# Kernel optimization log

Hardware: AMD Instinct MI355X
Metric: run time of the kernel (lower is better)

The kernel has to match this reference:

```python
import jax, jax.numpy as jnp
import numpy as np

H = W = 32
V = 1.5  # gaussian sigma used by the original _gussin(1.5)

def _gaussian_table():
    # gus[p, x, y] with p = i*32 + k, matching the original nested loops.
    r = np.arange(H, dtype=np.float64)
    d = (r[:, None, None, None] - r[None, None, :, None]) ** 2 \
        + (r[None, :, None, None] - r[None, None, None, :]) ** 2  # [i,k,x,y]
    g = np.exp(-d / (2.0 * V * V)) / (2.0 * np.pi * V * V)
    g = g.reshape(H * W, H, W)
    g = g / g.sum(axis=(1, 2), keepdims=True)  # per-position boundary normalization
    return jnp.asarray(g, dtype=jnp.float32)

_GUS = _gaussian_table()  # [1024, 32, 32]

def setup_inputs() -> dict:
    key = jax.random.key(0)
    ks = jax.random.split(key, 5)
    c, r = 1024, 16
    return {
        "x": jax.random.normal(ks[0], (1, c, H, W), jnp.float32),
        "se_w1": jax.random.normal(ks[1], (c // r, c), jnp.float32) * 0.03,
        "se_b1": jnp.zeros((c // r,), jnp.float32),
        "se_w2": jax.random.normal(ks[2], (c, c // r), jnp.float32) * 0.1,
        "se_b2": jnp.zeros((c,), jnp.float32),
        "conv_w": jax.random.normal(ks[3], (c, 2 * c), jnp.float32) * 0.02,
        "bn_gamma": jnp.ones((c,), jnp.float32),
        "bn_beta": jnp.zeros((c,), jnp.float32),
        "bn_mean": jnp.zeros((c,), jnp.float32),
        "bn_var": jnp.ones((c,), jnp.float32),
    }

def reference(x, se_w1, se_b1, se_w2, se_b2, conv_w, bn_gamma, bn_beta, bn_mean, bn_var):
    b, c, h, w = x.shape  # b == 1, h == w == 32 (hardcoded by the gaussian table)
    # ---- SE block ----
    y = x.mean(axis=(2, 3))                              # [b, c]
    y = jax.nn.relu(y @ se_w1.T + se_b1)                 # [b, c//r]
    y = jax.nn.sigmoid(y @ se_w2.T + se_b2)              # [b, c]
    x = x * y[:, :, None, None]
    # ---- gaussian spatial pooling (algebraic form of the O(H^2 W^2 C) expand) ----
    # x_spatial[c, p] = sum_{h,w} x[c,h,w] * gus[p,h,w]
    x_spatial = jnp.einsum('chw,phw->cp', x[0], _GUS).reshape(c, h, w)
    # ---- 3x3 local softmax attention on sigmoid features ----
    xr = jax.nn.sigmoid(x)                               # [1, c, h, w]
    xp = jnp.pad(xr, ((0, 0), (0, 0), (1, 1), (1, 1)))
    # torch F.unfold ordering: feature index = c_idx*9 + kh*3 + kw
    patches = jnp.stack([xp[:, :, i:i + h, j:j + w]
                         for i in range(3) for j in range(3)], axis=2)  # [1, c, 9, h, w]
    u = patches.reshape(c * 9, h * w).T                  # [hw, c*9]
    # faithful to the original reshape(hw, 3, 3, c) (reinterprets the c*9 layout)
    x3 = u.reshape(h * w, 3, 3, c)
    x1 = xr[0].transpose(1, 2, 0).reshape(h * w, 1, 1, c)
    logits = (x1 * x3).sum(-1).reshape(h * w, 9)         # [hw, 9]
    attn = jax.nn.softmax(logits, axis=1).reshape(h * w, 3, 3)
    x_range = jnp.einsum('pij,pijc->cp', attn, x3).reshape(c, h, w)
    # ---- fuse: 1x1 conv (no bias) + eval-mode BatchNorm + ReLU ----
    cat = jnp.concatenate([x_range, x_spatial], axis=0).reshape(b, 2 * c, h, w)
    out = jnp.einsum('oc,bchw->bohw', conv_w, cat)
    inv = jax.lax.rsqrt(bn_var + 1e-5)
    out = (out - bn_mean[None, :, None, None]) * (inv * bn_gamma)[None, :, None, None] \
          + bn_beta[None, :, None, None]
    return jax.nn.relu(out)
```

## Files before the change

kernel.cpp:

```cpp
#include <hip/hip_runtime.h>
#include <hip/hip_bf16.h>


typedef __attribute__((ext_vector_type(8))) short v8s;
typedef __attribute__((ext_vector_type(4))) float v4f;

__device__ __forceinline__ float sigmoidf_(float v) {
    return 1.f / (1.f + __expf(-v));
}
__device__ __forceinline__ unsigned short f2bf(float f) {
    unsigned u = __float_as_uint(f);
    u += 0x7fffu + ((u >> 16) & 1u);
    return (unsigned short)(u >> 16);
}
__device__ __forceinline__ float bf2f(unsigned short s) {
    return __uint_as_float(((unsigned)s) << 16);
}

__global__ __launch_bounds__(256) void k_A(const float* __restrict__ x,
                                           const float* __restrict__ W,
                                           float* __restrict__ mean,
                                           unsigned short* __restrict__ Wb,
                                           unsigned short* __restrict__ K2,
                                           unsigned short* __restrict__ xb) {
    __shared__ float Gs[32][32];
    int tid = threadIdx.x, bx = blockIdx.x;
    int wv = tid >> 6, lane = tid & 63;
    {
        int row = tid >> 3, col0 = (tid & 7) << 2;
        float e[4], s = 0.f;
        #pragma unroll
        for (int j = 0; j < 4; ++j) {
            float d = (float)(row - (col0 + j));
            e[j] = __expf(-d * d / 4.5f);
            s += e[j];
        }
        s += __shfl_xor(s, 4, 8);
        s += __shfl_xor(s, 2, 8);
        s += __shfl_xor(s, 1, 8);
        float is = 1.f / s;
        #pragma unroll
        for (int j = 0; j < 4; ++j) Gs[row][col0 + j] = e[j] * is;
    }
    #pragma unroll
    for (int k = 0; k < 8; ++k) {
        int e = (k << 18) + (bx << 10) + (tid << 2);
        float4 v = *(const float4*)(W + e);
        uint2 pk;
        pk.x = (unsigned)f2bf(v.x) | ((unsigned)f2bf(v.y) << 16);
        pk.y = (unsigned)f2bf(v.z) | ((unsigned)f2bf(v.w) << 16);
        *(uint2*)(Wb + e) = pk;
    }
    int c = (bx << 2) + wv;
    const float* xp = x + (size_t)c * 1024;
    float4 vj[4];
    float s = 0.f;
    #pragma unroll
    for (int j = 0; j < 4; ++j) {
        vj[j] = *(const float4*)(xp + (j << 8) + (lane << 2));
        s += vj[j].x + vj[j].y + vj[j].z + vj[j].w;
    }
    #pragma unroll
    for (int o = 32; o; o >>= 1) s += __shfl_down(s, o);
    if (lane == 0) mean[c] = s * (1.f / 1024.f);
    #pragma unroll
    for (int j = 0; j < 4; ++j) {
        uint2 pk;
        pk.x = (unsigned)f2bf(vj[j].x) | ((unsigned)f2bf(vj[j].y) << 16);
        pk.y = (unsigned)f2bf(vj[j].z) | ((unsigned)f2bf(vj[j].w) << 16);
        *(uint2*)(xb + (size_t)c * 1024 + (j << 8) + (lane << 2)) = pk;
    }
    __syncthreads();
    {
        int p = (bx << 2) + wv;
        float gr = Gs[p >> 5][lane >> 1];
        const float* gq = &Gs[p & 31][(lane & 1) << 4];
        unsigned pk[8];
        #pragma unroll
        for (int t = 0; t < 8; ++t) {
            float v0 = gr * gq[2 * t];
            float v1 = gr * gq[2 * t + 1];
            pk[t] = (unsigned)f2bf(v0) | ((unsigned)f2bf(v1) << 16);
        }
        unsigned short* dst = K2 + (size_t)p * 1024 + (lane << 4);
        *(uint4*)dst = *(uint4*)&pk[0];
        *(uint4*)(dst + 8) = *(uint4*)&pk[4];
    }
}

__global__ __launch_bounds__(256) void k_prep(const float* __restrict__ x,
                                              const float* __restrict__ mean,
                                              const float* __restrict__ w1,
                                              const float* __restrict__ b1,
                                              const float* __restrict__ w2,
                                              const float* __restrict__ b2,
                                              unsigned short* __restrict__ xrb,
                                              float* __restrict__ y2out) {
    __shared__ float ms[1024];
    __shared__ float y1s[64];
    __shared__ float y2s[64];
    __shared__ float T[64][65];
    int tid = threadIdx.x;
    int p0 = blockIdx.x << 6, c0 = blockIdx.y << 6;
    *(float4*)&ms[tid << 2] = *(const float4*)(mean + (tid << 2));
    __syncthreads();
    int wv = tid >> 6, lane = tid & 63;
    #pragma unroll
    for (int jj = 0; jj < 16; ++jj) {
        int j = (wv << 4) + jj;
        float s = 0.f;
        #pragma unroll
        for (int kk = 0; kk < 4; ++kk) {
            float4 wv4 = *(const float4*)(w1 + (size_t)j * 1024 + kk * 256 + (lane << 2));
            float4 mv  = *(const float4*)&ms[kk * 256 + (lane << 2)];
            s += wv4.x * mv.x + wv4.y * mv.y + wv4.z * mv.z + wv4.w * mv.w;
        }
        #pragma unroll
        for (int o = 32; o; o >>= 1) s += __shfl_down(s, o);
        if (lane == 0) y1s[j] = fmaxf(s + b1[j], 0.f);
    }
    __syncthreads();
    {
        int ci = tid >> 2, sub = tid & 3;
        float s = 0.f;
        const float* w2r = w2 + (size_t)(c0 + ci) * 64 + sub * 16;
        #pragma unroll
        for (int i = 0; i < 4; ++i) {
            float4 wv4 = *(const float4*)(w2r + (i << 2));
            float4 yv4 = *(const float4*)&y1s[sub * 16 + (i << 2)];
            s += wv4.x * yv4.x + wv4.y * yv4.y + wv4.z * yv4.z + wv4.w * yv4.w;
        }
        s += __shfl_down(s, 2, 4);
        s += __shfl_down(s, 1, 4);
        if (sub == 0) y2s[ci] = sigmoidf_(s + b2[c0 + ci]);
    }
    __syncthreads();
    if (blockIdx.x == 0 && tid < 64) y2out[c0 + tid] = y2s[tid];
    #pragma unroll
    for (int i = 0; i < 4; ++i) {
        int idx = tid + (i << 8);
        int row = idx >> 4;
        int col = (idx & 15) << 2;
        float sc = y2s[row];
        float4 v = *(const float4*)(x + (size_t)(c0 + row) * 1024 + p0 + col);
        T[col + 0][row] = sigmoidf_(v.x * sc);
        T[col + 1][row] = sigmoidf_(v.y * sc);
        T[col + 2][row] = sigmoidf_(v.z * sc);
        T[col + 3][row] = sigmoidf_(v.w * sc);
    }
    __syncthreads();
    #pragma unroll
    for (int i = 0; i < 4; ++i) {
        int idx = tid + (i << 8);
        int prow = idx >> 4;
        int cc = (idx & 15) << 2;
        uint2 pk;
        pk.x = (unsigned)f2bf(T[prow][cc + 0]) | ((unsigned)f2bf(T[prow][cc + 1]) << 16);
        pk.y = (unsigned)f2bf(T[prow][cc + 2]) | ((unsigned)f2bf(T[prow][cc + 3]) << 16);
        *(uint2*)(xrb + (size_t)(p0 + prow) * 1024 + c0 + cc) = pk;
    }
}

union __align__(16) SMem {
    struct { unsigned short As[64 * 72]; unsigned short Bs[64 * 72]; } sp;
    struct { unsigned short val[9216]; float part[9][4]; } at;
};

__global__ __launch_bounds__(256) void k_spattn(const unsigned short* __restrict__ xb,
                                                const unsigned short* __restrict__ xrb,
                                                const unsigned short* __restrict__ K2,
                                                const float* __restrict__ y2,
                                                unsigned short* __restrict__ Bt) {
    __shared__ SMem sm;
    int tid = threadIdx.x;
    int bx = blockIdx.x;
    int wv = tid >> 6, lane = tid & 63;
    if (bx < 256) {
        int wm = wv & 1, wn = wv >> 1;
        int m0 = (bx >> 4) << 6, n0 = (bx & 15) << 6;
        int col = lane & 15, quad = lane >> 4;
        int smi = tid >> 2;
        int sg = (tid & 3) * 2;
        v4f acc[2][2];
        #pragma unroll
        for (int i = 0; i < 2; ++i)
            #pragma unroll
            for (int j = 0; j < 2; ++j) acc[i][j] = (v4f){0.f, 0.f, 0.f, 0.f};
        const float4* pa = (const float4*)(K2 + (size_t)(m0 + smi) * 1024 + sg * 8);
        const float4* pb = (const float4*)(xb + (size_t)(n0 + smi) * 1024 + sg * 8);
        float4 ka0 = pa[0], ka1 = pa[1];
        float4 kb0 = pb[0], kb1 = pb[1];
        for (int it = 0; it < 16; ++it) {
            __syncthreads();
            *(float4*)&sm.sp.As[smi * 72 + sg * 8] = ka0;
            *(float4*)&sm.sp.As[smi * 72 + sg * 8 + 8] = ka1;
            *(float4*)&sm.sp.Bs[smi * 72 + sg * 8] = kb0;
            *(float4*)&sm.sp.Bs[smi * 72 + sg * 8 + 8] = kb1;
            __syncthreads();
            if (it + 1 < 16) {
                int k0 = (it + 1) << 6;
                pa = (const float4*)(K2 + (size_t)(m0 + smi) * 1024 + k0 + sg * 8);
                pb = (const float4*)(xb + (size_t)(n0 + smi) * 1024 + k0 + sg * 8);
                ka0 = pa[0]; ka1 = pa[1];
                kb0 = pb[0]; kb1 = pb[1];
            }
            #pragma unroll
            for (int ks = 0; ks < 2; ++ks) {
                int kg = ks * 4 + quad;
                int rA = wm * 32 + col;
                int rB = wn * 32 + col;
                v8s a0 = *(const v8s*)&sm.sp.As[rA * 72 + kg * 8];
                v8s a1 = *(const v8s*)&sm.sp.As[(rA + 16) * 72 + kg * 8];
                v8s b0 = *(const v8s*)&sm.sp.Bs[rB * 72 + kg * 8];
                v8s b1 = *(const v8s*)&sm.sp.Bs[(rB + 16) * 72 + kg * 8];
                acc[0][0] = __builtin_amdgcn_mfma_f32_16x16x32_bf16(a0, b0, acc[0][0], 0, 0, 0);
                acc[0][1] = __builtin_amdgcn_mfma_f32_16x16x32_bf16(a0, b1, acc[0][1], 0, 0, 0);
                acc[1][0] = __builtin_amdgcn_mfma_f32_16x16x32_bf16(a1, b0, acc[1][0], 0, 0, 0);
                acc[1][1] = __builtin_amdgcn_mfma_f32_16x16x32_bf16(a1, b1, acc[1][1], 0, 0, 0);
            }
        }
        #pragma unroll
        for (int mi = 0; mi < 2; ++mi)
            #pragma unroll
            for (int ni = 0; ni < 2; ++ni) {
                int mb = m0 + wm * 32 + mi * 16 + quad * 4;
                int nn = n0 + wn * 32 + ni * 16 + col;
                float yv = y2[nn];
                #pragma unroll
                for (int r = 0; r < 4; ++r)
                    Bt[(size_t)(mb + r) * 2048 + 1024 + nn] = f2bf(acc[mi][ni][r] * yv);
            }
    } else {
        int p = bx - 256;
        int h = p >> 5, w = p & 31;
        #pragma unroll
        for (int rem = 0; rem < 9; ++rem) {
            int dh = rem / 3 - 1, dw = rem % 3 - 1;
            bool ok = ((unsigned)(h + dh) < 32u) && ((unsigned)(w + dw) < 32u);
            const unsigned short* rp = xrb + (size_t)((h + dh) * 32 + (w + dw)) * 1024;
            #pragma unroll
            for (int j = 0; j < 4; ++j) {
                int cf = tid + (j << 8);
                sm.at.val[cf * 9 + rem] = ok ? rp[cf] : (unsigned short)0;
            }
        }
        __syncthreads();
        float ctr[4], vvq[9][4], lg[9];
        #pragma unroll
        for (int j = 0; j < 4; ++j) ctr[j] = bf2f(sm.at.val[(4 * tid + j) * 9 + 4]);
        #pragma unroll
        for (int q = 0; q < 9; ++q) {
            uint2 pk = *(const uint2*)&sm.at.val[(q << 10) + 4 * tid];
            vvq[q][0] = bf2f((unsigned short)(pk.x & 0xffffu));
            vvq[q][1] = bf2f((unsigned short)(pk.x >> 16));
            vvq[q][2] = bf2f((unsigned short)(pk.y & 0xffffu));
            vvq[q][3] = bf2f((unsigned short)(pk.y >> 16));
            lg[q] = ctr[0] * vvq[q][0] + ctr[1] * vvq[q][1]
                  + ctr[2] * vvq[q][2] + ctr[3] * vvq[q][3];
        }
        #pragma unroll
        for (int q = 0; q < 9; ++q) {
            float s = lg[q];
            #pragma unroll
            for (int o = 32; o; o >>= 1) s += __shfl_down(s, o);
            if (lane == 0) sm.at.part[q][wv] = s;
        }
        __syncthreads();
        float a9[9], mx = -3.4e38f;
        #pragma unroll
        for (int q = 0; q < 9; ++q) {
            a9[q] = sm.at.part[q][0] + sm.at.part[q][1] + sm.at.part[q][2] + sm.at.part[q][3];
            mx = fmaxf(mx, a9[q]);
        }
        float se = 0.f;
        #pragma unroll
        for (int q = 0; q < 9; ++q) { a9[q] = __expf(a9[q] - mx); se += a9[q]; }
        float inv = 1.f / se;
        float o4[4] = {0.f, 0.f, 0.f, 0.f};
        #pragma unroll
        for (int q = 0; q < 9; ++q) {
            float a = a9[q] * inv;
            #pragma unroll
            for (int j = 0; j < 4; ++j) o4[j] += a * vvq[q][j];
        }
        uint2 pk;
        pk.x = (unsigned)f2bf(o4[0]) | ((unsigned)f2bf(o4[1]) << 16);
        pk.y = (unsigned)f2bf(o4[2]) | ((unsigned)f2bf(o4[3]) << 16);
        *(uint2*)(Bt + (size_t)p * 2048 + 4 * tid) = pk;
    }
}

__global__ __launch_bounds__(512) void k_main(
    const unsigned short* __restrict__ A, const unsigned short* __restrict__ B,
    float* __restrict__ outF,
    const float* __restrict__ gamma, const float* __restrict__ beta,
    const float* __restrict__ mu, const float* __restrict__ var) {
    __shared__ unsigned short As[2][64 * 72];
    __shared__ unsigned short Bs[2][64 * 72];
    const int K = 2048;
    int tid = threadIdx.x;
    int wv = tid >> 6, lane = tid & 63;
    int wm = wv & 3, wn = wv >> 2;
    int m0 = blockIdx.y << 6, n0 = blockIdx.x << 6;
    int col = lane & 15, quad = lane >> 4;
    int srow = tid >> 3;
    int schunk = tid & 7;
    v4f acc[2];
    acc[0] = (v4f){0.f, 0.f, 0.f, 0.f};
    acc[1] = (v4f){0.f, 0.f, 0.f, 0.f};

    const float4* pa = (const float4*)(A + (size_t)(m0 + srow) * K + schunk * 8);
    const float4* pb = (const float4*)(B + (size_t)(n0 + srow) * K + schunk * 8);
    float4 ra = pa[0], rb = pb[0];
    *(float4*)&As[0][srow * 72 + schunk * 8] = ra;
    *(float4*)&Bs[0][srow * 72 + schunk * 8] = rb;
    for (int it = 0; it < 32; ++it) {
        __syncthreads();
        int cur = it & 1;
        if (it + 1 < 32) {
            int k0 = (it + 1) << 6;
            pa = (const float4*)(A + (size_t)(m0 + srow) * K + k0 + schunk * 8);
            pb = (const float4*)(B + (size_t)(n0 + srow) * K + k0 + schunk * 8);
            ra = pa[0]; rb = pb[0];
        }
        #pragma unroll
        for (int ks = 0; ks < 2; ++ks) {
            int kg = ks * 4 + quad;
            int rA = wm * 16 + col;
            int rB = wn * 32 + col;
            v8s a  = *(const v8s*)&As[cur][rA * 72 + kg * 8];
            v8s b0 = *(const v8s*)&Bs[cur][rB * 72 + kg * 8];
            v8s b1 = *(const v8s*)&Bs[cur][(rB + 16) * 72 + kg * 8];
            acc[0] = __builtin_amdgcn_mfma_f32_16x16x32_bf16(a, b0, acc[0], 0, 0, 0);
            acc[1] = __builtin_amdgcn_mfma_f32_16x16x32_bf16(a, b1, acc[1], 0, 0, 0);
        }
        if (it + 1 < 32) {
            int nxt = cur ^ 1;
            *(float4*)&As[nxt][srow * 72 + schunk * 8] = ra;
            *(float4*)&Bs[nxt][srow * 72 + schunk * 8] = rb;
        }
    }
    #pragma unroll
    for (int ni = 0; ni < 2; ++ni) {
        int mb = m0 + wm * 16 + quad * 4;
        int nn = n0 + wn * 32 + ni * 16 + col;
        #pragma unroll
        for (int r = 0; r < 4; ++r) {
            int mm = mb + r;
            float iv = rsqrtf(var[mm] + 1e-5f);
            float sc = iv * gamma[mm];
            float sh = beta[mm] - mu[mm] * sc;
            outF[((size_t)mm << 10) + nn] = fmaxf(fmaf(acc[ni][r], sc, sh), 0.f);
        }
    }
}

extern "C" void kernel_launch(void* const* d_in, const int* in_sizes, int n_in,
                              void* d_out, int out_size, void* d_ws, size_t ws_size,
                              hipStream_t stream) {
    const float* x     = (const float*)d_in[0];
    const float* w1    = (const float*)d_in[1];
    const float* b1    = (const float*)d_in[2];
    const float* w2    = (const float*)d_in[3];
    const float* b2    = (const float*)d_in[4];
    const float* cw    = (const float*)d_in[5];
    const float* gamma = (const float*)d_in[6];
    const float* beta  = (const float*)d_in[7];
    const float* mu    = (const float*)d_in[8];
    const float* var   = (const float*)d_in[9];
    float* wsf = (float*)d_ws;
    unsigned short* Wb  = (unsigned short*)wsf;
    unsigned short* Bt  = (unsigned short*)(wsf + (1 << 20));
    unsigned short* xrb = (unsigned short*)(wsf + (2 << 20));
    unsigned short* K2  = (unsigned short*)(wsf + (2 << 20) + (1 << 19));
    float* mean = wsf + (3 << 20);
    float* y2   = mean + 1024;
    unsigned short* xb = (unsigned short*)(y2 + 1024);
    float* out  = (float*)d_out;

    dim3 g16(16, 16);
    k_A     <<<256, 256, 0, stream>>>(x, cw, mean, Wb, K2, xb);
    k_prep  <<<g16, 256, 0, stream>>>(x, mean, w1, b1, w2, b2, xrb, y2);
    k_spattn<<<1280, 256, 0, stream>>>(xb, xrb, K2, y2, Bt);
    k_main  <<<g16, 512, 0, stream>>>(Wb, Bt, out, gamma, beta, mu, var);
}
```

Before: 129.7 us.

## Replace dense gaussian pooling GEMM with separable 1D blur via small MFMAs

The gaussian table is separable (G[i,x]*G[k,y]), so spatial pooling becomes two 32x32 matrix products per channel, G·X·Gᵀ, computed with MFMA in k_A. This replaces the 1024x1024x1024 GEMM against the K2 table. The SE scale is applied afterwards in k_prep while transposing into Bt, and attention moves into its own kernel. BN scale and shift are precomputed once, and k_main gets an XCD-aware block remap. The intermediate is rounded to bf16 twice, which may slightly change accuracy.

```diff
diff --git a/kernel.cpp b/kernel.cpp
--- a/kernel.cpp
+++ b/kernel.cpp
@@ -19,11 +19,18 @@
 
 __global__ __launch_bounds__(256) void k_A(const float* __restrict__ x,
                                            const float* __restrict__ W,
+                                           const float* __restrict__ gamma,
+                                           const float* __restrict__ beta,
+                                           const float* __restrict__ mu,
+                                           const float* __restrict__ var,
                                            float* __restrict__ mean,
                                            unsigned short* __restrict__ Wb,
-                                           unsigned short* __restrict__ K2,
-                                           unsigned short* __restrict__ xb) {
-    __shared__ float Gs[32][32];
+                                           unsigned short* __restrict__ U,
+                                           float* __restrict__ bnsc,
+                                           float* __restrict__ bnsh) {
+    __shared__ unsigned short Gb[32 * 48];
+    __shared__ unsigned short Xs[4][32 * 48];
+    __shared__ unsigned short Ts[4][32 * 48];
     int tid = threadIdx.x, bx = blockIdx.x;
     int wv = tid >> 6, lane = tid & 63;
     {
@@ -39,8 +46,10 @@
         s += __shfl_xor(s, 2, 8);
         s += __shfl_xor(s, 1, 8);
         float is = 1.f / s;
-        #pragma unroll
-        for (int j = 0; j < 4; ++j) Gs[row][col0 + j] = e[j] * is;
+        uint2 pk;
+        pk.x = (unsigned)f2bf(e[0] * is) | ((unsigned)f2bf(e[1] * is) << 16);
+        pk.y = (unsigned)f2bf(e[2] * is) | ((unsigned)f2bf(e[3] * is) << 16);
+        *(uint2*)&Gb[row * 48 + col0] = pk;
     }
     #pragma unroll
     for (int k = 0; k < 8; ++k) {
@@ -52,6 +61,12 @@
         *(uint2*)(Wb + e) = pk;
     }
     int c = (bx << 2) + wv;
+    if (lane == 0) {
+        float iv = rsqrtf(var[c] + 1e-5f);
+        float sc = iv * gamma[c];
+        bnsc[c] = sc;
+        bnsh[c] = beta[c] - mu[c] * sc;
+    }
     const float* xp = x + (size_t)c * 1024;
     float4 vj[4];
     float s = 0.f;
@@ -65,27 +80,58 @@
     if (lane == 0) mean[c] = s * (1.f / 1024.f);
     #pragma unroll
     for (int j = 0; j < 4; ++j) {
+        int h = (j << 3) + (lane >> 3);
+        int w0 = (lane & 7) << 2;
         uint2 pk;
         pk.x = (unsigned)f2bf(vj[j].x) | ((unsigned)f2bf(vj[j].y) << 16);
         pk.y = (unsigned)f2bf(vj[j].z) | ((unsigned)f2bf(vj[j].w) << 16);
-        *(uint2*)(xb + (size_t)c * 1024 + (j << 8) + (lane << 2)) = pk;
-    }
-    __syncthreads();
-    {
-        int p = (bx << 2) + wv;
-        float gr = Gs[p >> 5][lane >> 1];
-        const float* gq = &Gs[p & 31][(lane & 1) << 4];
-        unsigned pk[8];
-        #pragma unroll
-        for (int t = 0; t < 8; ++t) {
-            float v0 = gr * gq[2 * t];
-            float v1 = gr * gq[2 * t + 1];
-            pk[t] = (unsigned)f2bf(v0) | ((unsigned)f2bf(v1) << 16);
-        }
-        unsigned short* dst = K2 + (size_t)p * 1024 + (lane << 4);
-        *(uint4*)dst = *(uint4*)&pk[0];
-        *(uint4*)(dst + 8) = *(uint4*)&pk[4];
-    }
+        *(uint2*)&Xs[wv][h * 48 + w0] = pk;
+    }
+    __syncthreads();
+    int colf = lane & 15, quad = lane >> 4;
+    v8s ga[2], xbv[2];
+    #pragma unroll
+    for (int mi = 0; mi < 2; ++mi)
+        ga[mi] = *(const v8s*)&Gb[(mi * 16 + colf) * 48 + quad * 8];
+    #pragma unroll
+    for (int ni = 0; ni < 2; ++ni)
+        xbv[ni] = *(const v8s*)&Xs[wv][(ni * 16 + colf) * 48 + quad * 8];
+    v4f c1[2][2];
+    #pragma unroll
+    for (int mi = 0; mi < 2; ++mi)
+        #pragma unroll
+        for (int ni = 0; ni < 2; ++ni) {
+            c1[mi][ni] = (v4f){0.f, 0.f, 0.f, 0.f};
+            c1[mi][ni] = __builtin_amdgcn_mfma_f32_16x16x32_bf16(ga[mi], xbv[ni], c1[mi][ni], 0, 0, 0);
+        }
+    #pragma unroll
+    for (int mi = 0; mi < 2; ++mi)
+        #pragma unroll
+        for (int ni = 0; ni < 2; ++ni)
+            #pragma unroll
+            for (int r = 0; r < 4; ++r)
+                Ts[wv][(mi * 16 + quad * 4 + r) * 48 + ni * 16 + colf] = f2bf(c1[mi][ni][r]);
+    __syncthreads();
+    v8s tb[2];
+    #pragma unroll
+    for (int ni = 0; ni < 2; ++ni)
+        tb[ni] = *(const v8s*)&Ts[wv][(ni * 16 + colf) * 48 + quad * 8];
+    v4f c2[2][2];
+    #pragma unroll
+    for (int mi = 0; mi < 2; ++mi)
+        #pragma unroll
+        for (int ni = 0; ni < 2; ++ni) {
+            c2[mi][ni] = (v4f){0.f, 0.f, 0.f, 0.f};
+            c2[mi][ni] = __builtin_amdgcn_mfma_f32_16x16x32_bf16(ga[mi], tb[ni], c2[mi][ni], 0, 0, 0);
+        }
+    #pragma unroll
+    for (int mi = 0; mi < 2; ++mi)
+        #pragma unroll
+        for (int ni = 0; ni < 2; ++ni)
+            #pragma unroll
+            for (int r = 0; r < 4; ++r)
+                U[(size_t)c * 1024 + (mi * 16 + quad * 4 + r) * 32 + ni * 16 + colf] =
+                    f2bf(c2[mi][ni][r]);
 }
 
 __global__ __launch_bounds__(256) void k_prep(const float* __restrict__ x,
@@ -94,8 +140,9 @@
                                               const float* __restrict__ b1,
                                               const float* __restrict__ w2,
                                               const float* __restrict__ b2,
+                                              const unsigned short* __restrict__ U,
                                               unsigned short* __restrict__ xrb,
-                                              float* __restrict__ y2out) {
+                                              unsigned short* __restrict__ Bt) {
     __shared__ float ms[1024];
     __shared__ float y1s[64];
     __shared__ float y2s[64];
@@ -135,7 +182,6 @@
         if (sub == 0) y2s[ci] = sigmoidf_(s + b2[c0 + ci]);
     }
     __syncthreads();
-    if (blockIdx.x == 0 && tid < 64) y2out[c0 + tid] = y2s[tid];
     #pragma unroll
     for (int i = 0; i < 4; ++i) {
         int idx = tid + (i << 8);
@@ -159,149 +205,117 @@
         pk.y = (unsigned)f2bf(T[prow][cc + 2]) | ((unsigned)f2bf(T[prow][cc + 3]) << 16);
         *(uint2*)(xrb + (size_t)(p0 + prow) * 1024 + c0 + cc) = pk;
     }
-}
-
-union __align__(16) SMem {
-    struct { unsigned short As[64 * 72]; unsigned short Bs[64 * 72]; } sp;
-    struct { unsigned short val[9216]; float part[9][4]; } at;
-};
-
-__global__ __launch_bounds__(256) void k_spattn(const unsigned short* __restrict__ xb,
-                                                const unsigned short* __restrict__ xrb,
-                                                const unsigned short* __restrict__ K2,
-                                                const float* __restrict__ y2,
-                                                unsigned short* __restrict__ Bt) {
-    __shared__ SMem sm;
+    __syncthreads();
+    #pragma unroll
+    for (int i = 0; i < 4; ++i) {
+        int idx = tid + (i << 8);
+        int row = idx >> 4;
+        int col = (idx & 15) << 2;
+        float sc = y2s[row];
+        uint2 pk = *(const uint2*)(U + (size_t)(c0 + row) * 1024 + p0 + col);
+        T[col + 0][row] = bf2f((unsigned short)(pk.x & 0xffffu)) * sc;
+        T[col + 1][row] = bf2f((unsigned short)(pk.x >> 16)) * sc;
+        T[col + 2][row] = bf2f((unsigned short)(pk.y & 0xffffu)) * sc;
+        T[col + 3][row] = bf2f((unsigned short)(pk.y >> 16)) * sc;
+    }
+    __syncthreads();
+    #pragma unroll
+    for (int i = 0; i < 4; ++i) {
+        int idx = tid + (i << 8);
+        int prow = idx >> 4;
+        int cc = (idx & 15) << 2;
+        uint2 pk;
+        pk.x = (unsigned)f2bf(T[prow][cc + 0]) | ((unsigned)f2bf(T[prow][cc + 1]) << 16);
+        pk.y = (unsigned)f2bf(T[prow][cc + 2]) | ((unsigned)f2bf(T[prow][cc + 3]) << 16);
+        *(uint2*)(Bt + (size_t)(p0 + prow) * 2048 + 1024 + c0 + cc) = pk;
+    }
+}
+
+__global__ __launch_bounds__(256) void k_attn(const unsigned short* __restrict__ xrb,
+                                              unsigned short* __restrict__ Bt) {
+    __shared__ struct { unsigned short val[9216]; float part[9][4]; } sm;
     int tid = threadIdx.x;
-    int bx = blockIdx.x;
+    int p = blockIdx.x;
     int wv = tid >> 6, lane = tid & 63;
-    if (bx < 256) {
-        int wm = wv & 1, wn = wv >> 1;
-        int m0 = (bx >> 4) << 6, n0 = (bx & 15) << 6;
-        int col = lane & 15, quad = lane >> 4;
-        int smi = tid >> 2;
-        int sg = (tid & 3) * 2;
-        v4f acc[2][2];
-        #pragma unroll
-        for (int i = 0; i < 2; ++i)
-            #pragma unroll
-            for (int j = 0; j < 2; ++j) acc[i][j] = (v4f){0.f, 0.f, 0.f, 0.f};
-        const float4* pa = (const float4*)(K2 + (size_t)(m0 + smi) * 1024 + sg * 8);
-        const float4* pb = (const float4*)(xb + (size_t)(n0 + smi) * 1024 + sg * 8);
-        float4 ka0 = pa[0], ka1 = pa[1];
-        float4 kb0 = pb[0], kb1 = pb[1];
-        for (int it = 0; it < 16; ++it) {
-            __syncthreads();
-            *(float4*)&sm.sp.As[smi * 72 + sg * 8] = ka0;
-            *(float4*)&sm.sp.As[smi * 72 + sg * 8 + 8] = ka1;
-            *(float4*)&sm.sp.Bs[smi * 72 + sg * 8] = kb0;
-            *(float4*)&sm.sp.Bs[smi * 72 + sg * 8 + 8] = kb1;
-            __syncthreads();
-            if (it + 1 < 16) {
-                int k0 = (it + 1) << 6;
-                pa = (const float4*)(K2 + (size_t)(m0 + smi) * 1024 + k0 + sg * 8);
-                pb = (const float4*)(xb + (size_t)(n0 + smi) * 1024 + k0 + sg * 8);
-                ka0 = pa[0]; ka1 = pa[1];
-                kb0 = pb[0]; kb1 = pb[1];
-            }
-            #pragma unroll
-            for (int ks = 0; ks < 2; ++ks) {
-                int kg = ks * 4 + quad;
-                int rA = wm * 32 + col;
-                int rB = wn * 32 + col;
-                v8s a0 = *(const v8s*)&sm.sp.As[rA * 72 + kg * 8];
-                v8s a1 = *(const v8s*)&sm.sp.As[(rA + 16) * 72 + kg * 8];
-                v8s b0 = *(const v8s*)&sm.sp.Bs[rB * 72 + kg * 8];
-                v8s b1 = *(const v8s*)&sm.sp.Bs[(rB + 16) * 72 + kg * 8];
-                acc[0][0] = __builtin_amdgcn_mfma_f32_16x16x32_bf16(a0, b0, acc[0][0], 0, 0, 0);
-                acc[0][1] = __builtin_amdgcn_mfma_f32_16x16x32_bf16(a0, b1, acc[0][1], 0, 0, 0);
-                acc[1][0] = __builtin_amdgcn_mfma_f32_16x16x32_bf16(a1, b0, acc[1][0], 0, 0, 0);
-                acc[1][1] = __builtin_amdgcn_mfma_f32_16x16x32_bf16(a1, b1, acc[1][1], 0, 0, 0);
-            }
-        }
-        #pragma unroll
-        for (int mi = 0; mi < 2; ++mi)
-            #pragma unroll
-            for (int ni = 0; ni < 2; ++ni) {
-                int mb = m0 + wm * 32 + mi * 16 + quad * 4;
-                int nn = n0 + wn * 32 + ni * 16 + col;
-                float yv = y2[nn];
-                #pragma unroll
-                for (int r = 0; r < 4; ++r)
-                    Bt[(size_t)(mb + r) * 2048 + 1024 + nn] = f2bf(acc[mi][ni][r] * yv);
-            }
-    } else {
-        int p = bx - 256;
-        int h = p >> 5, w = p & 31;
-        #pragma unroll
-        for (int rem = 0; rem < 9; ++rem) {
-            int dh = rem / 3 - 1, dw = rem % 3 - 1;
-            bool ok = ((unsigned)(h + dh) < 32u) && ((unsigned)(w + dw) < 32u);
-            const unsigned short* rp = xrb + (size_t)((h + dh) * 32 + (w + dw)) * 1024;
-            #pragma unroll
-            for (int j = 0; j < 4; ++j) {
-                int cf = tid + (j << 8);
-                sm.at.val[cf * 9 + rem] = ok ? rp[cf] : (unsigned short)0;
-            }
-        }
-        __syncthreads();
-        float ctr[4], vvq[9][4], lg[9];
-        #pragma unroll
-        for (int j = 0; j < 4; ++j) ctr[j] = bf2f(sm.at.val[(4 * tid + j) * 9 + 4]);
-        #pragma unroll
-        for (int q = 0; q < 9; ++q) {
-            uint2 pk = *(const uint2*)&sm.at.val[(q << 10) + 4 * tid];
-            vvq[q][0] = bf2f((unsigned short)(pk.x & 0xffffu));
-            vvq[q][1] = bf2f((unsigned short)(pk.x >> 16));
-            vvq[q][2] = bf2f((unsigned short)(pk.y & 0xffffu));
-            vvq[q][3] = bf2f((unsigned short)(pk.y >> 16));
-            lg[q] = ctr[0] * vvq[q][0] + ctr[1] * vvq[q][1]
-                  + ctr[2] * vvq[q][2] + ctr[3] * vvq[q][3];
-        }
-        #pragma unroll
-        for (int q = 0; q < 9; ++q) {
-            float s = lg[q];
-            #pragma unroll
-            for (int o = 32; o; o >>= 1) s += __shfl_down(s, o);
-            if (lane == 0) sm.at.part[q][wv] = s;
-        }
-        __syncthreads();
-        float a9[9], mx = -3.4e38f;
-        #pragma unroll
-        for (int q = 0; q < 9; ++q) {
-            a9[q] = sm.at.part[q][0] + sm.at.part[q][1] + sm.at.part[q][2] + sm.at.part[q][3];
-            mx = fmaxf(mx, a9[q]);
-        }
-        float se = 0.f;
-        #pragma unroll
-        for (int q = 0; q < 9; ++q) { a9[q] = __expf(a9[q] - mx); se += a9[q]; }
-        float inv = 1.f / se;
-        float o4[4] = {0.f, 0.f, 0.f, 0.f};
-        #pragma unroll
-        for (int q = 0; q < 9; ++q) {
-            float a = a9[q] * inv;
-            #pragma unroll
-            for (int j = 0; j < 4; ++j) o4[j] += a * vvq[q][j];
-        }
-        uint2 pk;
-        pk.x = (unsigned)f2bf(o4[0]) | ((unsigned)f2bf(o4[1]) << 16);
-        pk.y = (unsigned)f2bf(o4[2]) | ((unsigned)f2bf(o4[3]) << 16);
-        *(uint2*)(Bt + (size_t)p * 2048 + 4 * tid) = pk;
-    }
+    int h = p >> 5, w = p & 31;
+    float ctr[4];
+    #pragma unroll
+    for (int rem = 0; rem < 9; ++rem) {
+        int dh = rem / 3 - 1, dw = rem % 3 - 1;
+        bool ok = ((unsigned)(h + dh) < 32u) && ((unsigned)(w + dw) < 32u);
+        uint2 v = make_uint2(0u, 0u);
+        if (ok)
+            v = *(const uint2*)(xrb + (size_t)((h + dh) * 32 + (w + dw)) * 1024 + 4 * tid);
+        unsigned short e0 = (unsigned short)(v.x & 0xffffu);
+        unsigned short e1 = (unsigned short)(v.x >> 16);
+        unsigned short e2 = (unsigned short)(v.y & 0xffffu);
+        unsigned short e3 = (unsigned short)(v.y >> 16);
+        sm.val[(4 * tid + 0) * 9 + rem] = e0;
+        sm.val[(4 * tid + 1) * 9 + rem] = e1;
+        sm.val[(4 * tid + 2) * 9 + rem] = e2;
+        sm.val[(4 * tid + 3) * 9 + rem] = e3;
+        if (rem == 4) {
+            ctr[0] = bf2f(e0); ctr[1] = bf2f(e1); ctr[2] = bf2f(e2); ctr[3] = bf2f(e3);
+        }
+    }
+    __syncthreads();
+    float vvq[9][4], lg[9];
+    #pragma unroll
+    for (int q = 0; q < 9; ++q) {
+        uint2 pk = *(const uint2*)&sm.val[(q << 10) + 4 * tid];
+        vvq[q][0] = bf2f((unsigned short)(pk.x & 0xffffu));
+        vvq[q][1] = bf2f((unsigned short)(pk.x >> 16));
+        vvq[q][2] = bf2f((unsigned short)(pk.y & 0xffffu));
+        vvq[q][3] = bf2f((unsigned short)(pk.y >> 16));
+        lg[q] = ctr[0] * vvq[q][0] + ctr[1] * vvq[q][1]
+              + ctr[2] * vvq[q][2] + ctr[3] * vvq[q][3];
+    }
+    #pragma unroll
+    for (int q = 0; q < 9; ++q) {
+        float s = lg[q];
+        #pragma unroll
+        for (int o = 32; o; o >>= 1) s += __shfl_down(s, o);
+        if (lane == 0) sm.part[q][wv] = s;
+    }
+    __syncthreads();
+    float a9[9], mx = -3.4e38f;
+    #pragma unroll
+    for (int q = 0; q < 9; ++q) {
+        a9[q] = sm.part[q][0] + sm.part[q][1] + sm.part[q][2] + sm.part[q][3];
+        mx = fmaxf(mx, a9[q]);
+    }
+    float se = 0.f;
+    #pragma unroll
+    for (int q = 0; q < 9; ++q) { a9[q] = __expf(a9[q] - mx); se += a9[q]; }
+    float inv = 1.f / se;
+    float o4[4] = {0.f, 0.f, 0.f, 0.f};
+    #pragma unroll
+    for (int q = 0; q < 9; ++q) {
+        float a = a9[q] * inv;
+        #pragma unroll
+        for (int j = 0; j < 4; ++j) o4[j] += a * vvq[q][j];
+    }
+    uint2 pk;
+    pk.x = (unsigned)f2bf(o4[0]) | ((unsigned)f2bf(o4[1]) << 16);
+    pk.y = (unsigned)f2bf(o4[2]) | ((unsigned)f2bf(o4[3]) << 16);
+    *(uint2*)(Bt + (size_t)p * 2048 + 4 * tid) = pk;
 }
 
 __global__ __launch_bounds__(512) void k_main(
     const unsigned short* __restrict__ A, const unsigned short* __restrict__ B,
     float* __restrict__ outF,
-    const float* __restrict__ gamma, const float* __restrict__ beta,
-    const float* __restrict__ mu, const float* __restrict__ var) {
+    const float* __restrict__ bnsc, const float* __restrict__ bnsh) {
     __shared__ unsigned short As[2][64 * 72];
     __shared__ unsigned short Bs[2][64 * 72];
     const int K = 2048;
     int tid = threadIdx.x;
+    int bid = blockIdx.x;
+    int xcd = bid & 7, idx = bid >> 3;
+    int by = ((xcd >> 1) << 2) + (idx >> 3);
+    int bxn = ((xcd & 1) << 3) + (idx & 7);
+    int m0 = by << 6, n0 = bxn << 6;
     int wv = tid >> 6, lane = tid & 63;
     int wm = wv & 3, wn = wv >> 2;
-    int m0 = blockIdx.y << 6, n0 = blockIdx.x << 6;
     int col = lane & 15, quad = lane >> 4;
     int srow = tid >> 3;
     int schunk = tid & 7;
@@ -347,9 +361,8 @@
         #pragma unroll
         for (int r = 0; r < 4; ++r) {
             int mm = mb + r;
-            float iv = rsqrtf(var[mm] + 1e-5f);
-            float sc = iv * gamma[mm];
-            float sh = beta[mm] - mu[mm] * sc;
+            float sc = bnsc[mm];
+            float sh = bnsh[mm];
             outF[((size_t)mm << 10) + nn] = fmaxf(fmaf(acc[ni][r], sc, sh), 0.f);
         }
     }
@@ -372,15 +385,14 @@
     unsigned short* Wb  = (unsigned short*)wsf;
     unsigned short* Bt  = (unsigned short*)(wsf + (1 << 20));
     unsigned short* xrb = (unsigned short*)(wsf + (2 << 20));
-    unsigned short* K2  = (unsigned short*)(wsf + (2 << 20) + (1 << 19));
+    unsigned short* U   = (unsigned short*)(wsf + (2 << 20) + (1 << 19));
     float* mean = wsf + (3 << 20);
-    float* y2   = mean + 1024;
-    unsigned short* xb = (unsigned short*)(y2 + 1024);
+    float* bnsc = mean + 1024;
+    float* bnsh = mean + 2048;
     float* out  = (float*)d_out;
 
-    dim3 g16(16, 16);
-    k_A     <<<256, 256, 0, stream>>>(x, cw, mean, Wb, K2, xb);
-    k_prep  <<<g16, 256, 0, stream>>>(x, mean, w1, b1, w2, b2, xrb, y2);
-    k_spattn<<<1280, 256, 0, stream>>>(xb, xrb, K2, y2, Bt);
-    k_main  <<<g16, 512, 0, stream>>>(Wb, Bt, out, gamma, beta, mu, var);
-}
+    k_A    <<<256, 256, 0, stream>>>(x, cw, gamma, beta, mu, var, mean, Wb, U, bnsc, bnsh);
+    k_prep <<<dim3(16, 16), 256, 0, stream>>>(x, mean, w1, b1, w2, b2, U, xrb, Bt);
+    k_attn <<<1024, 256, 0, stream>>>(xrb, Bt);
+    k_main <<<256, 512, 0, stream>>>(Wb, Bt, out, bnsc, bnsh);
+}
```

Measured after the change: 123.0 us. 5.2% less time.
